# Kernel optimization log

Measured on AMD Instinct MI355X. Metric: run time of the kernel, lower is better.

## Reference

```python
import jax, jax.numpy as jnp
import numpy as np

N_RES = 2_000_000
N_DOM = 2
B_WIN = 100
S_STRIDE = 10
HIDDEN = 128


def _build_windows():
    # Faithful port of the __init__ index construction.
    nb_per_res = B_WIN // S_STRIDE
    balance = B_WIN - S_STRIDE + 1
    start = np.maximum(np.arange(N_RES) + balance - B_WIN, 0)
    start = start // S_STRIDE + (start % S_STRIDE != 0).astype(np.int64)
    bs = start[:, None] + np.arange(nb_per_res)[None, :]
    return bs.astype(np.int32)


def setup_inputs() -> dict:
    key = jax.random.key(0)
    ks = jax.random.split(key, 7)
    bs_per_res = _build_windows()
    nb_windows = int(bs_per_res[-1, -1]) + 1  # 200009
    # weights near 1 (original inits to ones) so products stay well-scaled
    weights = jax.random.uniform(ks[0], (nb_windows, N_DOM), minval=0.5, maxval=1.5, dtype=jnp.float32)
    latent_variables = jax.random.normal(ks[1], (6,), dtype=jnp.float32)
    features = jax.random.normal(ks[2], (2, 50), dtype=jnp.float32)  # replaces torch.randn((2,50))
    W1 = jax.random.normal(ks[3], (53, HIDDEN), dtype=jnp.float32) * 0.1
    b1 = jnp.zeros((HIDDEN,), dtype=jnp.float32)
    W2 = jax.random.normal(ks[4], (HIDDEN, 3), dtype=jnp.float32) * 0.1
    b2 = jnp.zeros((3,), dtype=jnp.float32)
    local_frame = jax.random.normal(ks[5], (3, 3), dtype=jnp.float32)
    atom_absolute_positions = jax.random.normal(ks[6], (3 * N_RES, 3), dtype=jnp.float32)
    return {
        'weights': weights,
        'latent_variables': latent_variables,
        'features': features,
        'W1': W1, 'b1': b1, 'W2': W2, 'b2': b2,
        'local_frame': local_frame,
        'atom_absolute_positions': atom_absolute_positions,
        'bs_per_res': jnp.asarray(bs_per_res),
    }


def multiply_windows_weights(weights, bs_per_res):
    # gather: (N_res, nb_per_res, N_dom); product over the window axis, softmax over domains
    gathered = weights[bs_per_res]
    weights_per_residue = jnp.prod(gathered, axis=1)
    return jax.nn.softmax(weights_per_residue, axis=1)


def reference(weights, latent_variables, features, W1, b1, W2, b2,
              local_frame, atom_absolute_positions, bs_per_res):
    attn = multiply_windows_weights(weights, bs_per_res)  # (N_res, N_dom)
    # features_and_latent: (2, 53)
    fl = jnp.concatenate([features, latent_variables.reshape(2, 3)], axis=1)
    h = jax.nn.relu(fl @ W1 + b1)
    scalars_per_domain = h @ W2 + b2  # (N_dom, 3)
    # deform_structure: note module stores local_frame transposed
    translation_vectors = scalars_per_domain @ local_frame.T  # (N_dom, 3)
    translation_per_residue = attn @ translation_vectors      # (N_res, 3)
    new_atom_positions = atom_absolute_positions + jnp.repeat(translation_per_residue, 3, axis=0)
    return new_atom_positions, attn, translation_per_residue
```

## Files before the change

### kernel.cpp

```cpp
#include <hip/hip_runtime.h>

#define N_RES   2000000
#define HIDDEN  128
#define BLK     256
#define NTILES  7813
#define GRID    2048

typedef float f32x4 __attribute__((ext_vector_type(4)));
typedef float f32x2 __attribute__((ext_vector_type(2)));

__global__ __launch_bounds__(BLK) void fused_kernel(
    const float* __restrict__ weights,
    const float* __restrict__ latent,
    const float* __restrict__ features,
    const float* __restrict__ W1,
    const float* __restrict__ b1,
    const float* __restrict__ W2,
    const float* __restrict__ b2,
    const float* __restrict__ lf,
    const float* __restrict__ pos,
    float* __restrict__ out_pos,
    float* __restrict__ out_attn,
    float* __restrict__ out_trans)
{
    __shared__ float h[2][HIDDEN];
    __shared__ float sv[6];
    __shared__ float tvs[6];
    __shared__ __align__(16) float t_lds[2][3 * BLK];

    const int tid = threadIdx.x;

    {
        const int d = tid >> 7, j = tid & 127;
        float acc = b1[j];
        #pragma unroll
        for (int k = 0; k < 50; ++k)
            acc += features[d * 50 + k] * W1[k * HIDDEN + j];
        #pragma unroll
        for (int k = 0; k < 3; ++k)
            acc += latent[d * 3 + k] * W1[(50 + k) * HIDDEN + j];
        h[d][j] = fmaxf(acc, 0.0f);
    }
    __syncthreads();
    {
        const int dd   = tid >> 7;
        const int rest = tid & 127;
        const int c    = rest >> 5;
        const int l    = rest & 31;
        if (c < 3) {
            float a = 0.f;
            #pragma unroll
            for (int m = 0; m < 4; ++m)
                a += h[dd][l + 32 * m] * W2[(l + 32 * m) * 3 + c];
            #pragma unroll
            for (int off = 16; off >= 1; off >>= 1)
                a += __shfl_xor(a, off, 64);
            if (l == 0) sv[dd * 3 + c] = a + b2[c];
        }
    }
    __syncthreads();
    if (tid < 6) {
        const int dd = tid / 3, c = tid % 3;
        float a = 0.f;
        #pragma unroll
        for (int k = 0; k < 3; ++k)
            a += sv[dd * 3 + k] * lf[c * 3 + k];
        tvs[tid] = a;
    }
    __syncthreads();

    const float tv0 = tvs[0], tv1 = tvs[1], tv2 = tvs[2];
    const float tv3 = tvs[3], tv4 = tvs[4], tv5 = tvs[5];

    int buf = 0;
    for (int tile = blockIdx.x; tile < NTILES; tile += GRID, buf ^= 1) {
        const int r0   = tile * BLK;
        const int r    = r0 + tid;
        const int nres = min(BLK, N_RES - r0);
        const int nch  = (9 * nres) >> 2;

        const float4* __restrict__ pos4 = (const float4*)(pos + 9ll * r0);
        float4 pA = make_float4(0.f, 0.f, 0.f, 0.f);
        float4 pB = pA, pC = pA;
        if (tid            < nch) pA = pos4[tid];
        if (tid +     BLK  < nch) pB = pos4[tid + BLK];
        if (tid + 2 * BLK  < nch) pC = pos4[tid + 2 * BLK];

        float t0 = 0.f, t1 = 0.f, t2 = 0.f;
        if (r < N_RES) {
            const int raw   = max(r - 9, 0);
            const int start = (raw + 9) / 10;
            const float2* wbase = (const float2*)(weights) + start;
            float p0 = 1.0f, p1 = 1.0f;
            #pragma unroll
            for (int j = 0; j < 10; ++j) {
                const float2 w = wbase[j];
                p0 *= w.x;
                p1 *= w.y;
            }
            const float m   = fmaxf(p0, p1);
            const float e0  = __expf(p0 - m);
            const float e1  = __expf(p1 - m);
            const float inv = 1.0f / (e0 + e1);
            const float a0  = e0 * inv;
            const float a1  = e1 * inv;

            f32x2 av; av.x = a0; av.y = a1;
            __builtin_nontemporal_store(av, (f32x2*)out_attn + r);

            t0 = a0 * tv0 + a1 * tv3;
            t1 = a0 * tv1 + a1 * tv4;
            t2 = a0 * tv2 + a1 * tv5;
        }
        float* __restrict__ tl = t_lds[buf];
        tl[3 * tid + 0] = t0;
        tl[3 * tid + 1] = t1;
        tl[3 * tid + 2] = t2;
        __syncthreads();

        const int ntr = (3 * nres) >> 2;
        if (tid < ntr)
            __builtin_nontemporal_store(((const f32x4*)tl)[tid],
                                        (f32x4*)(out_trans + 3ll * r0) + tid);

        f32x4* __restrict__ o4 = (f32x4*)(out_pos + 9ll * r0);
        auto addt = [&](float4 v, int c) -> f32x4 {
            float* vp = (float*)&v;
            const int e = 4 * c;
            int rl = e / 9;
            int cm = e - 9 * rl;
            #pragma unroll
            for (int k = 0; k < 4; ++k) {
                const int c3 = (cm >= 6) ? cm - 6 : ((cm >= 3) ? cm - 3 : cm);
                vp[k] += tl[3 * rl + c3];
                if (++cm == 9) { cm = 0; ++rl; }
            }
            f32x4 rv; rv.x = v.x; rv.y = v.y; rv.z = v.z; rv.w = v.w;
            return rv;
        };
        if (tid            < nch)
            __builtin_nontemporal_store(addt(pA, tid          ), o4 + tid          );
        if (tid +     BLK  < nch)
            __builtin_nontemporal_store(addt(pB, tid +     BLK), o4 + tid +     BLK);
        if (tid + 2 * BLK  < nch)
            __builtin_nontemporal_store(addt(pC, tid + 2 * BLK), o4 + tid + 2 * BLK);
    }
}

extern "C" void kernel_launch(void* const* d_in, const int* in_sizes, int n_in,
                              void* d_out, int out_size, void* d_ws, size_t ws_size,
                              hipStream_t stream) {
    const float* weights  = (const float*)d_in[0];
    const float* latent   = (const float*)d_in[1];
    const float* features = (const float*)d_in[2];
    const float* W1       = (const float*)d_in[3];
    const float* b1       = (const float*)d_in[4];
    const float* W2       = (const float*)d_in[5];
    const float* b2       = (const float*)d_in[6];
    const float* lf       = (const float*)d_in[7];
    const float* pos      = (const float*)d_in[8];

    float* out = (float*)d_out;

    fused_kernel<<<GRID, BLK, 0, stream>>>(
        weights, latent, features, W1, b1, W2, b2, lf, pos,
        out,
        out + 18000000,
        out + 22000000);
}
```

Before: 234.9 us.

## Split fused kernel into attention kernel and position streaming kernel

Splits the single fused kernel into two launches. The first computes attention and per-residue translations and writes them with plain stores. The second streams the atom positions and adds translations read back from global memory (likely L2-resident). This removes the per-tile LDS staging and block barriers, and lets the streaming kernel run with one thread per float4 across many blocks. The cost is a second launch and an extra read of the 24 MB translation array.

```diff
diff --git a/kernel.cpp b/kernel.cpp
--- a/kernel.cpp
+++ b/kernel.cpp
@@ -3,13 +3,12 @@
 #define N_RES   2000000
 #define HIDDEN  128
 #define BLK     256
-#define NTILES  7813
-#define GRID    2048
+#define GRID1   2048
+#define NCH4    4500000
 
 typedef float f32x4 __attribute__((ext_vector_type(4)));
-typedef float f32x2 __attribute__((ext_vector_type(2)));
 
-__global__ __launch_bounds__(BLK) void fused_kernel(
+__global__ __launch_bounds__(BLK) void attn_kernel(
     const float* __restrict__ weights,
     const float* __restrict__ latent,
     const float* __restrict__ features,
@@ -18,15 +17,12 @@
     const float* __restrict__ W2,
     const float* __restrict__ b2,
     const float* __restrict__ lf,
-    const float* __restrict__ pos,
-    float* __restrict__ out_pos,
     float* __restrict__ out_attn,
     float* __restrict__ out_trans)
 {
     __shared__ float h[2][HIDDEN];
     __shared__ float sv[6];
     __shared__ float tvs[6];
-    __shared__ __align__(16) float t_lds[2][3 * BLK];
 
     const int tid = threadIdx.x;
 
@@ -72,79 +68,55 @@
     const float tv0 = tvs[0], tv1 = tvs[1], tv2 = tvs[2];
     const float tv3 = tvs[3], tv4 = tvs[4], tv5 = tvs[5];
 
-    int buf = 0;
-    for (int tile = blockIdx.x; tile < NTILES; tile += GRID, buf ^= 1) {
-        const int r0   = tile * BLK;
-        const int r    = r0 + tid;
-        const int nres = min(BLK, N_RES - r0);
-        const int nch  = (9 * nres) >> 2;
+    for (int r = blockIdx.x * BLK + tid; r < N_RES; r += GRID1 * BLK) {
+        const int raw   = max(r - 9, 0);
+        const int start = (raw + 9) / 10;
+        const float2* wbase = (const float2*)(weights) + start;
+        float p0 = 1.0f, p1 = 1.0f;
+        #pragma unroll
+        for (int j = 0; j < 10; ++j) {
+            const float2 w = wbase[j];
+            p0 *= w.x;
+            p1 *= w.y;
+        }
+        const float m   = fmaxf(p0, p1);
+        const float e0  = __expf(p0 - m);
+        const float e1  = __expf(p1 - m);
+        const float inv = 1.0f / (e0 + e1);
+        const float a0  = e0 * inv;
+        const float a1  = e1 * inv;
 
-        const float4* __restrict__ pos4 = (const float4*)(pos + 9ll * r0);
-        float4 pA = make_float4(0.f, 0.f, 0.f, 0.f);
-        float4 pB = pA, pC = pA;
-        if (tid            < nch) pA = pos4[tid];
-        if (tid +     BLK  < nch) pB = pos4[tid + BLK];
-        if (tid + 2 * BLK  < nch) pC = pos4[tid + 2 * BLK];
+        ((float2*)out_attn)[r] = make_float2(a0, a1);
 
-        float t0 = 0.f, t1 = 0.f, t2 = 0.f;
-        if (r < N_RES) {
-            const int raw   = max(r - 9, 0);
-            const int start = (raw + 9) / 10;
-            const float2* wbase = (const float2*)(weights) + start;
-            float p0 = 1.0f, p1 = 1.0f;
-            #pragma unroll
-            for (int j = 0; j < 10; ++j) {
-                const float2 w = wbase[j];
-                p0 *= w.x;
-                p1 *= w.y;
-            }
-            const float m   = fmaxf(p0, p1);
-            const float e0  = __expf(p0 - m);
-            const float e1  = __expf(p1 - m);
-            const float inv = 1.0f / (e0 + e1);
-            const float a0  = e0 * inv;
-            const float a1  = e1 * inv;
+        out_trans[3 * r + 0] = a0 * tv0 + a1 * tv3;
+        out_trans[3 * r + 1] = a0 * tv1 + a1 * tv4;
+        out_trans[3 * r + 2] = a0 * tv2 + a1 * tv5;
+    }
+}
 
-            f32x2 av; av.x = a0; av.y = a1;
-            __builtin_nontemporal_store(av, (f32x2*)out_attn + r);
+__global__ __launch_bounds__(BLK) void stream_kernel(
+    const float* __restrict__ pos,
+    const float* __restrict__ trans,
+    float* __restrict__ out_pos)
+{
+    const int j = blockIdx.x * BLK + threadIdx.x;
+    if (j >= NCH4) return;
 
-            t0 = a0 * tv0 + a1 * tv3;
-            t1 = a0 * tv1 + a1 * tv4;
-            t2 = a0 * tv2 + a1 * tv5;
-        }
-        float* __restrict__ tl = t_lds[buf];
-        tl[3 * tid + 0] = t0;
-        tl[3 * tid + 1] = t1;
-        tl[3 * tid + 2] = t2;
-        __syncthreads();
+    float4 v = ((const float4*)pos)[j];
 
-        const int ntr = (3 * nres) >> 2;
-        if (tid < ntr)
-            __builtin_nontemporal_store(((const f32x4*)tl)[tid],
-                                        (f32x4*)(out_trans + 3ll * r0) + tid);
+    const int e = 4 * j;
+    int rl = e / 9;
+    int cm = e - 9 * rl;
+    float* vp = (float*)&v;
+    #pragma unroll
+    for (int k = 0; k < 4; ++k) {
+        const int c3 = (cm >= 6) ? cm - 6 : ((cm >= 3) ? cm - 3 : cm);
+        vp[k] += trans[3 * rl + c3];
+        if (++cm == 9) { cm = 0; ++rl; }
+    }
 
-        f32x4* __restrict__ o4 = (f32x4*)(out_pos + 9ll * r0);
-        auto addt = [&](float4 v, int c) -> f32x4 {
-            float* vp = (float*)&v;
-            const int e = 4 * c;
-            int rl = e / 9;
-            int cm = e - 9 * rl;
-            #pragma unroll
-            for (int k = 0; k < 4; ++k) {
-                const int c3 = (cm >= 6) ? cm - 6 : ((cm >= 3) ? cm - 3 : cm);
-                vp[k] += tl[3 * rl + c3];
-                if (++cm == 9) { cm = 0; ++rl; }
-            }
-            f32x4 rv; rv.x = v.x; rv.y = v.y; rv.z = v.z; rv.w = v.w;
-            return rv;
-        };
-        if (tid            < nch)
-            __builtin_nontemporal_store(addt(pA, tid          ), o4 + tid          );
-        if (tid +     BLK  < nch)
-            __builtin_nontemporal_store(addt(pB, tid +     BLK), o4 + tid +     BLK);
-        if (tid + 2 * BLK  < nch)
-            __builtin_nontemporal_store(addt(pC, tid + 2 * BLK), o4 + tid + 2 * BLK);
-    }
+    f32x4 rv; rv.x = v.x; rv.y = v.y; rv.z = v.z; rv.w = v.w;
+    __builtin_nontemporal_store(rv, (f32x4*)out_pos + j);
 }
 
 extern "C" void kernel_launch(void* const* d_in, const int* in_sizes, int n_in,
@@ -160,11 +132,15 @@
     const float* lf       = (const float*)d_in[7];
     const float* pos      = (const float*)d_in[8];
 
-    float* out = (float*)d_out;
+    float* out       = (float*)d_out;
+    float* out_pos   = out;
+    float* out_attn  = out + 18000000;
+    float* out_trans = out + 22000000;
 
-    fused_kernel<<<GRID, BLK, 0, stream>>>(
-        weights, latent, features, W1, b1, W2, b2, lf, pos,
-        out,
-        out + 18000000,
-        out + 22000000);
+    attn_kernel<<<GRID1, BLK, 0, stream>>>(
+        weights, latent, features, W1, b1, W2, b2, lf,
+        out_attn, out_trans);
+
+    const int blocks = (NCH4 + BLK - 1) / BLK;
+    stream_kernel<<<blocks, BLK, 0, stream>>>(pos, out_trans, out_pos);
 }
```

Result: no change. 232.9 us (-0.9%).
